# Optimization experiments

Hardware: AMD Instinct MI355X
Metric: run time of the kernel (lower is better)

Reference implementation:

```python
import jax, jax.numpy as jnp
import numpy as np

V = 500000        # total elements
S = 50000         # num samples (segments)
D = 128           # input = hidden = output size


def setup_inputs() -> dict:
    key = jax.random.key(0)
    k1, k2, k3, k4, k5 = jax.random.split(key, 5)
    scale = 1.0 / np.sqrt(D)
    return {
        "element_embeddings": jax.random.normal(k1, (V, D), dtype=jnp.float32),
        "element_to_sample_map": jnp.sort(jax.random.randint(k2, (V,), 0, S)),
        "num_samples": S,
        "Wq": jax.random.normal(k3, (D, D), dtype=jnp.float32) * scale,
        "Wk": jax.random.normal(k4, (D, D), dtype=jnp.float32) * scale,
        "Wo": jax.random.normal(k5, (D, D), dtype=jnp.float32) * scale,
    }


def reference(element_embeddings, element_to_sample_map, num_samples, Wq, Wk, Wo):
    x = element_embeddings                    # [V, D]
    idx = element_to_sample_map               # [V] int

    # --- query summarizer: linear projection + segment mean ---
    q_elem = x @ Wq.T                          # [V, H]
    q_sum = jax.ops.segment_sum(q_elem, idx, num_segments=num_samples)   # [S, H]
    counts = jax.ops.segment_sum(jnp.ones((x.shape[0],), x.dtype), idx,
                                 num_segments=num_samples)               # [S]
    queries = q_sum / jnp.maximum(counts, 1.0)[:, None]                  # [S, H]

    # --- attention scores: gather query per element, dot with key ---
    keys = x @ Wk.T                            # [V, H]
    queries_all = queries[idx]                 # [V, H] gather
    scores = jnp.einsum('vh,vh->v', queries_all, keys)                   # [V]

    # --- segment softmax (exp of scatter_log_softmax, eps=0) ---
    seg_max = jax.ops.segment_max(scores, idx, num_segments=num_samples) # [S]
    shifted = scores - seg_max[idx]
    e = jnp.exp(shifted)
    denom = jax.ops.segment_sum(e, idx, num_segments=num_samples)        # [S]
    probs = e / denom[idx]                                               # [V]

    # --- weighted scatter-sum of output projections ---
    out_elem = (x @ Wo.T) * probs[:, None]     # [V, D_out]
    return jax.ops.segment_sum(out_elem, idx, num_segments=num_samples)  # [S, D_out]
```

## Files before the change

kernel.cpp:

```cpp
#include <hip/hip_runtime.h>
#include <math.h>

#define D 128

__global__ void k_prep(const float* __restrict__ Wq, const float* __restrict__ Wk,
                       const float* __restrict__ Wo, float* __restrict__ M,
                       float* __restrict__ WoT) {
  int j = blockIdx.x, k = threadIdx.x;
  float acc = 0.f;
#pragma unroll 8
  for (int i = 0; i < D; ++i) acc = fmaf(Wq[i * D + j], Wk[i * D + k], acc);
  M[j * D + k] = acc;
  WoT[j * D + k] = Wo[k * D + j];
}

__global__ void k_starts(const int* __restrict__ idx, int* __restrict__ starts,
                         int V, int S) {
  int v = blockIdx.x * blockDim.x + threadIdx.x;
  if (v >= V) return;
  int c = idx[v];
  int p = (v == 0) ? -1 : idx[v - 1];
  for (int s = p + 1; s <= c; ++s) starts[s] = v;
  if (v == V - 1) {
    for (int s = c + 1; s <= S; ++s) starts[s] = V;
  }
}

__global__ void k_means(const float* __restrict__ x, const int* __restrict__ starts,
                        float* __restrict__ mean, int S) {
  int tid = blockIdx.x * blockDim.x + threadIdx.x;
  if (tid >= S * 32) return;
  int s = tid >> 5, g = tid & 31;
  int b = starts[s], e = starts[s + 1];
  float4 a = make_float4(0.f, 0.f, 0.f, 0.f);
  const float* xp = x + (size_t)b * D + g * 4;
  for (int v = b; v < e; ++v, xp += D) {
    float4 xv = *(const float4*)xp;
    a.x += xv.x; a.y += xv.y; a.z += xv.z; a.w += xv.w;
  }
  float inv = (e > b) ? 1.f / (float)(e - b) : 0.f;
  a.x *= inv; a.y *= inv; a.z *= inv; a.w *= inv;
  *(float4*)(mean + (size_t)s * D + g * 4) = a;
}

__global__ void k_rowmat4(const float* __restrict__ in, const float* __restrict__ B,
                          float* __restrict__ out, int S) {
  __shared__ float Bl[D * D];
  for (int i = threadIdx.x; i < D * D / 4; i += (int)blockDim.x)
    ((float4*)Bl)[i] = ((const float4*)B)[i];
  __syncthreads();
  int t = blockIdx.x * blockDim.x + threadIdx.x;
  int g = t & 31;
  int s0 = (t >> 5) * 4;
  if (s0 >= S) return;
  int nr = S - s0; nr = nr > 4 ? 4 : nr;
  float4 a0 = make_float4(0, 0, 0, 0), a1 = a0, a2 = a0, a3 = a0;
  const float4* r0 = (const float4*)(in + (size_t)s0 * D);
  const float4* r1 = (const float4*)(in + (size_t)(s0 + 1) * D);
  const float4* r2 = (const float4*)(in + (size_t)(s0 + 2) * D);
  const float4* r3 = (const float4*)(in + (size_t)(s0 + 3) * D);
#pragma unroll 4
  for (int j4 = 0; j4 < D / 4; ++j4) {
    float4 b0 = *(const float4*)(Bl + (j4 * 4 + 0) * D + g * 4);
    float4 b1 = *(const float4*)(Bl + (j4 * 4 + 1) * D + g * 4);
    float4 b2 = *(const float4*)(Bl + (j4 * 4 + 2) * D + g * 4);
    float4 b3 = *(const float4*)(Bl + (j4 * 4 + 3) * D + g * 4);
#define ROWFMA(ar, rr)                                                   \
    {                                                                    \
      float4 m = rr[j4];                                                 \
      ar.x = fmaf(m.x, b0.x, ar.x); ar.y = fmaf(m.x, b0.y, ar.y);        \
      ar.z = fmaf(m.x, b0.z, ar.z); ar.w = fmaf(m.x, b0.w, ar.w);        \
      ar.x = fmaf(m.y, b1.x, ar.x); ar.y = fmaf(m.y, b1.y, ar.y);        \
      ar.z = fmaf(m.y, b1.z, ar.z); ar.w = fmaf(m.y, b1.w, ar.w);        \
      ar.x = fmaf(m.z, b2.x, ar.x); ar.y = fmaf(m.z, b2.y, ar.y);        \
      ar.z = fmaf(m.z, b2.z, ar.z); ar.w = fmaf(m.z, b2.w, ar.w);        \
      ar.x = fmaf(m.w, b3.x, ar.x); ar.y = fmaf(m.w, b3.y, ar.y);        \
      ar.z = fmaf(m.w, b3.z, ar.z); ar.w = fmaf(m.w, b3.w, ar.w);        \
    }
    ROWFMA(a0, r0);
    if (nr > 1) ROWFMA(a1, r1);
    if (nr > 2) ROWFMA(a2, r2);
    if (nr > 3) ROWFMA(a3, r3);
#undef ROWFMA
  }
  *(float4*)(out + (size_t)s0 * D + g * 4) = a0;
  if (nr > 1) *(float4*)(out + (size_t)(s0 + 1) * D + g * 4) = a1;
  if (nr > 2) *(float4*)(out + (size_t)(s0 + 2) * D + g * 4) = a2;
  if (nr > 3) *(float4*)(out + (size_t)(s0 + 3) * D + g * 4) = a3;
}

__global__ void k_score_y(const float* __restrict__ x, const int* __restrict__ starts,
                          const float* __restrict__ t, float* __restrict__ y, int S) {
  int tid = blockIdx.x * blockDim.x + threadIdx.x;
  if (tid >= S * 32) return;
  int s = tid >> 5, g = tid & 31;
  int b = starts[s], e = starts[s + 1];
  float4 t4 = *(const float4*)(t + (size_t)s * D + g * 4);
  float4 a = make_float4(0.f, 0.f, 0.f, 0.f);
  float den = 0.f;
  const float* xp = x + (size_t)b * D + g * 4;
  for (int v = b; v < e; ++v, xp += D) {
    float4 xv = *(const float4*)xp;
    float p = t4.x * xv.x + t4.y * xv.y + t4.z * xv.z + t4.w * xv.w;
    p += __shfl_xor(p, 16);
    p += __shfl_xor(p, 8);
    p += __shfl_xor(p, 4);
    p += __shfl_xor(p, 2);
    p += __shfl_xor(p, 1);
    float w = __expf(p);
    den += w;
    a.x = fmaf(w, xv.x, a.x); a.y = fmaf(w, xv.y, a.y);
    a.z = fmaf(w, xv.z, a.z); a.w = fmaf(w, xv.w, a.w);
  }
  float inv = (den > 0.f) ? 1.f / den : 0.f;
  a.x *= inv; a.y *= inv; a.z *= inv; a.w *= inv;
  *(float4*)(y + (size_t)s * D + g * 4) = a;
}

extern "C" void kernel_launch(void* const* d_in, const int* in_sizes, int n_in,
                              void* d_out, int out_size, void* d_ws, size_t ws_size,
                              hipStream_t stream) {
  const float* x = (const float*)d_in[0];
  const int* idx = (const int*)d_in[1];
  const float* Wq = (const float*)d_in[3];
  const float* Wk = (const float*)d_in[4];
  const float* Wo = (const float*)d_in[5];
  float* out = (float*)d_out;
  const int V = in_sizes[1];
  const int S = out_size / D;

  char* ws = (char*)d_ws;
  float* M = (float*)(ws + 0);
  float* WoT = (float*)(ws + 65536);
  int* starts = (int*)(ws + 131072);
  size_t base = (131072 + 4 * (size_t)(S + 1) + 255) & ~(size_t)255;
  size_t segbytes = (size_t)S * D * 4;
  float* mean = (float*)(ws + base);
  float* y = mean;
  float* t = (float*)(ws + base + segbytes);

  hipLaunchKernelGGL(k_prep, dim3(D), dim3(D), 0, stream, Wq, Wk, Wo, M, WoT);
  hipLaunchKernelGGL(k_starts, dim3((V + 255) / 256), dim3(256), 0, stream, idx, starts, V, S);
  hipLaunchKernelGGL(k_means, dim3((S * 32 + 255) / 256), dim3(256), 0, stream, x, starts, mean, S);
  hipLaunchKernelGGL(k_rowmat4, dim3(((S + 3) / 4 * 32 + 255) / 256), dim3(256), 0, stream, mean, M, t, S);
  hipLaunchKernelGGL(k_score_y, dim3((S * 32 + 255) / 256), dim3(256), 0, stream, x, starts, t, y, S);
  hipLaunchKernelGGL(k_rowmat4, dim3(((S + 3) / 4 * 32 + 255) / 256), dim3(256), 0, stream, y, WoT, out, S);
}
```

Baseline: 273.2 us.

## Replace per-segment reduction kernels with element-tiled shared-memory segment sums

The per-segment kernels (one 32-lane group per segment looping over its elements) become an element-tiled kernel. Each block takes 64 consecutive rows, reduces them into shared-memory bins per segment, then writes interior segments directly and boundary segments with global atomics. Normalisation by count or softmax denominator moves into the epilogue of the row-matrix kernel, and a zeroing kernel is added for the accumulators. The aim is to remove the load imbalance and poor occupancy of variable-length segment loops. In exchange it adds atomics, an extra zeroing pass, and drops the max-shift from the softmax as before.

New measurement: 418.7 us. 1.53x slower.

```diff
diff --git a/kernel.cpp b/kernel.cpp
--- a/kernel.cpp
+++ b/kernel.cpp
@@ -2,6 +2,8 @@
 #include <math.h>
 
 #define D 128
+#define TR 64
+#define TPB 256
 
 __global__ void k_prep(const float* __restrict__ Wq, const float* __restrict__ Wk,
                        const float* __restrict__ Wo, float* __restrict__ M,
@@ -26,25 +28,139 @@
   }
 }
 
-__global__ void k_means(const float* __restrict__ x, const int* __restrict__ starts,
-                        float* __restrict__ mean, int S) {
-  int tid = blockIdx.x * blockDim.x + threadIdx.x;
-  if (tid >= S * 32) return;
-  int s = tid >> 5, g = tid & 31;
-  int b = starts[s], e = starts[s + 1];
-  float4 a = make_float4(0.f, 0.f, 0.f, 0.f);
-  const float* xp = x + (size_t)b * D + g * 4;
-  for (int v = b; v < e; ++v, xp += D) {
-    float4 xv = *(const float4*)xp;
-    a.x += xv.x; a.y += xv.y; a.z += xv.z; a.w += xv.w;
-  }
-  float inv = (e > b) ? 1.f / (float)(e - b) : 0.f;
-  a.x *= inv; a.y *= inv; a.z *= inv; a.w *= inv;
-  *(float4*)(mean + (size_t)s * D + g * 4) = a;
-}
-
+__global__ void k_zero(float4* __restrict__ p, long long nf4) {
+  long long i = (long long)blockIdx.x * blockDim.x + threadIdx.x;
+  long long st = (long long)gridDim.x * blockDim.x;
+  float4 z = make_float4(0.f, 0.f, 0.f, 0.f);
+  for (; i < nf4; i += st) p[i] = z;
+}
+
+template <int PASS>
+__global__ __launch_bounds__(TPB) void k_segsum(
+    const float* __restrict__ x, const int* __restrict__ idx,
+    const float* __restrict__ t, float* __restrict__ gout,
+    float* __restrict__ gden, int V) {
+  __shared__ float bsum[TR * D];
+  __shared__ float bden[TR];
+  __shared__ int brank[TR];
+  __shared__ int bseg[TR];
+  __shared__ int bnb;
+
+  const int tid = threadIdx.x;
+  const int wave = tid >> 6;
+  const int lane = tid & 63;
+  const int gl = lane & 31;
+  const int half = lane >> 5;
+  const int v0 = blockIdx.x * TR;
+  const int nrows = min(TR, V - v0);
+
+  if (wave == 0) {
+    int l = lane;
+    int seg = idx[v0 + min(l, nrows - 1)];
+    int prev = __shfl_up(seg, 1);
+    bool flag = (l > 0) && (l < nrows) && (seg != prev);
+    unsigned long long bal = __ballot(flag);
+    int rank = __popcll(bal << (63 - l));
+    brank[l] = rank;
+    if (l == 0 || flag) bseg[rank] = seg;
+    if (l == 63) bnb = rank + 1;
+  }
+  __syncthreads();
+  const int nb = bnb;
+  for (int i = tid; i < nb * D; i += TPB) bsum[i] = 0.f;
+  if (PASS == 2) {
+    for (int i = tid; i < nb; i += TPB) bden[i] = 0.f;
+  }
+  __syncthreads();
+
+  const int r0 = wave * 16 + half;
+
+  float4 xr[8];
+#pragma unroll
+  for (int i = 0; i < 8; ++i) {
+    int rv = v0 + min(r0 + 2 * i, nrows - 1);
+    xr[i] = *(const float4*)(x + (size_t)rv * D + gl * 4);
+  }
+
+  int curRank = brank[r0];
+  float4 t4 = make_float4(0.f, 0.f, 0.f, 0.f);
+  if (PASS == 2) {
+    int seg = bseg[curRank];
+    t4 = *(const float4*)(t + (size_t)seg * D + gl * 4);
+  }
+  float4 acc = make_float4(0.f, 0.f, 0.f, 0.f);
+  float dacc = 0.f;
+
+#pragma unroll
+  for (int i = 0; i < 8; ++i) {
+    int r = r0 + 2 * i;
+    bool valid = (r < nrows);
+    int rk = brank[min(r, TR - 1)];
+    if (rk != curRank) {
+      float* bp = bsum + curRank * D + gl * 4;
+      unsafeAtomicAdd(bp + 0, acc.x);
+      unsafeAtomicAdd(bp + 1, acc.y);
+      unsafeAtomicAdd(bp + 2, acc.z);
+      unsafeAtomicAdd(bp + 3, acc.w);
+      if (PASS == 2 && gl == 0) unsafeAtomicAdd(&bden[curRank], dacc);
+      acc = make_float4(0.f, 0.f, 0.f, 0.f);
+      dacc = 0.f;
+      curRank = rk;
+      if (PASS == 2) {
+        int seg = bseg[rk];
+        t4 = *(const float4*)(t + (size_t)seg * D + gl * 4);
+      }
+    }
+    float w = valid ? 1.f : 0.f;
+    if (PASS == 2) {
+      float4 xv = xr[i];
+      float p = t4.x * xv.x + t4.y * xv.y + t4.z * xv.z + t4.w * xv.w;
+      p += __shfl_xor(p, 16);
+      p += __shfl_xor(p, 8);
+      p += __shfl_xor(p, 4);
+      p += __shfl_xor(p, 2);
+      p += __shfl_xor(p, 1);
+      w = valid ? __expf(p) : 0.f;
+      dacc += w;
+    }
+    acc.x = fmaf(w, xr[i].x, acc.x);
+    acc.y = fmaf(w, xr[i].y, acc.y);
+    acc.z = fmaf(w, xr[i].z, acc.z);
+    acc.w = fmaf(w, xr[i].w, acc.w);
+  }
+  {
+    float* bp = bsum + curRank * D + gl * 4;
+    unsafeAtomicAdd(bp + 0, acc.x);
+    unsafeAtomicAdd(bp + 1, acc.y);
+    unsafeAtomicAdd(bp + 2, acc.z);
+    unsafeAtomicAdd(bp + 3, acc.w);
+    if (PASS == 2 && gl == 0) unsafeAtomicAdd(&bden[curRank], dacc);
+  }
+  __syncthreads();
+
+  for (int i = tid; i < nb * D; i += TPB) {
+    int b = i >> 7;
+    int c = i & (D - 1);
+    int seg = bseg[b];
+    float val = bsum[i];
+    float* gp = gout + (size_t)seg * D + c;
+    if (b == 0 || b == nb - 1) unsafeAtomicAdd(gp, val);
+    else *gp = val;
+  }
+  if (PASS == 2) {
+    for (int b = tid; b < nb; b += TPB) {
+      int seg = bseg[b];
+      if (b == 0 || b == nb - 1) unsafeAtomicAdd(gden + seg, bden[b]);
+      else gden[seg] = bden[b];
+    }
+  }
+}
+
+template <int MODE>
 __global__ void k_rowmat4(const float* __restrict__ in, const float* __restrict__ B,
-                          float* __restrict__ out, int S) {
+                          float* __restrict__ out, int S,
+                          const int* __restrict__ starts,
+                          const float* __restrict__ den) {
   __shared__ float Bl[D * D];
   for (int i = threadIdx.x; i < D * D / 4; i += (int)blockDim.x)
     ((float4*)Bl)[i] = ((const float4*)B)[i];
@@ -53,7 +169,8 @@
   int g = t & 31;
   int s0 = (t >> 5) * 4;
   if (s0 >= S) return;
-  int nr = S - s0; nr = nr > 4 ? 4 : nr;
+  int nr = S - s0;
+  nr = nr > 4 ? 4 : nr;
   float4 a0 = make_float4(0, 0, 0, 0), a1 = a0, a2 = a0, a3 = a0;
   const float4* r0 = (const float4*)(in + (size_t)s0 * D);
   const float4* r1 = (const float4*)(in + (size_t)(s0 + 1) * D);
@@ -83,38 +200,26 @@
     if (nr > 3) ROWFMA(a3, r3);
 #undef ROWFMA
   }
+  float sc[4];
+#pragma unroll
+  for (int k = 0; k < 4; ++k) {
+    int s = s0 + (k < nr ? k : 0);
+    if (MODE == 0) {
+      int n = starts[s + 1] - starts[s];
+      sc[k] = 1.f / (float)(n > 1 ? n : 1);
+    } else {
+      float dn = den[s];
+      sc[k] = (dn > 0.f) ? 1.f / dn : 0.f;
+    }
+  }
+  a0.x *= sc[0]; a0.y *= sc[0]; a0.z *= sc[0]; a0.w *= sc[0];
+  a1.x *= sc[1]; a1.y *= sc[1]; a1.z *= sc[1]; a1.w *= sc[1];
+  a2.x *= sc[2]; a2.y *= sc[2]; a2.z *= sc[2]; a2.w *= sc[2];
+  a3.x *= sc[3]; a3.y *= sc[3]; a3.z *= sc[3]; a3.w *= sc[3];
   *(float4*)(out + (size_t)s0 * D + g * 4) = a0;
   if (nr > 1) *(float4*)(out + (size_t)(s0 + 1) * D + g * 4) = a1;
   if (nr > 2) *(float4*)(out + (size_t)(s0 + 2) * D + g * 4) = a2;
   if (nr > 3) *(float4*)(out + (size_t)(s0 + 3) * D + g * 4) = a3;
-}
-
-__global__ void k_score_y(const float* __restrict__ x, const int* __restrict__ starts,
-                          const float* __restrict__ t, float* __restrict__ y, int S) {
-  int tid = blockIdx.x * blockDim.x + threadIdx.x;
-  if (tid >= S * 32) return;
-  int s = tid >> 5, g = tid & 31;
-  int b = starts[s], e = starts[s + 1];
-  float4 t4 = *(const float4*)(t + (size_t)s * D + g * 4);
-  float4 a = make_float4(0.f, 0.f, 0.f, 0.f);
-  float den = 0.f;
-  const float* xp = x + (size_t)b * D + g * 4;
-  for (int v = b; v < e; ++v, xp += D) {
-    float4 xv = *(const float4*)xp;
-    float p = t4.x * xv.x + t4.y * xv.y + t4.z * xv.z + t4.w * xv.w;
-    p += __shfl_xor(p, 16);
-    p += __shfl_xor(p, 8);
-    p += __shfl_xor(p, 4);
-    p += __shfl_xor(p, 2);
-    p += __shfl_xor(p, 1);
-    float w = __expf(p);
-    den += w;
-    a.x = fmaf(w, xv.x, a.x); a.y = fmaf(w, xv.y, a.y);
-    a.z = fmaf(w, xv.z, a.z); a.w = fmaf(w, xv.w, a.w);
-  }
-  float inv = (den > 0.f) ? 1.f / den : 0.f;
-  a.x *= inv; a.y *= inv; a.z *= inv; a.w *= inv;
-  *(float4*)(y + (size_t)s * D + g * 4) = a;
 }
 
 extern "C" void kernel_launch(void* const* d_in, const int* in_sizes, int n_in,
@@ -134,15 +239,20 @@
   float* WoT = (float*)(ws + 65536);
   int* starts = (int*)(ws + 131072);
   size_t base = (131072 + 4 * (size_t)(S + 1) + 255) & ~(size_t)255;
-  size_t segbytes = (size_t)S * D * 4;
-  float* mean = (float*)(ws + base);
-  float* y = mean;
-  float* t = (float*)(ws + base + segbytes);
+  float* qsum = (float*)(ws + base);
+  float* ysum = qsum + (size_t)S * D;
+  float* den = ysum + (size_t)S * D;
+  long long zf4 = ((long long)S * (2 * D + 1)) / 4;
+  size_t tbase = (base + (size_t)S * (2 * D + 1) * 4 + 255) & ~(size_t)255;
+  float* t = (float*)(ws + tbase);
+
+  const int NT = (V + TR - 1) / TR;
 
   hipLaunchKernelGGL(k_prep, dim3(D), dim3(D), 0, stream, Wq, Wk, Wo, M, WoT);
   hipLaunchKernelGGL(k_starts, dim3((V + 255) / 256), dim3(256), 0, stream, idx, starts, V, S);
-  hipLaunchKernelGGL(k_means, dim3((S * 32 + 255) / 256), dim3(256), 0, stream, x, starts, mean, S);
-  hipLaunchKernelGGL(k_rowmat4, dim3(((S + 3) / 4 * 32 + 255) / 256), dim3(256), 0, stream, mean, M, t, S);
-  hipLaunchKernelGGL(k_score_y, dim3((S * 32 + 255) / 256), dim3(256), 0, stream, x, starts, t, y, S);
-  hipLaunchKernelGGL(k_rowmat4, dim3(((S + 3) / 4 * 32 + 255) / 256), dim3(256), 0, stream, y, WoT, out, S);
-}
+  hipLaunchKernelGGL(k_zero, dim3(2048), dim3(256), 0, stream, (float4*)qsum, zf4);
+  hipLaunchKernelGGL((k_segsum<1>), dim3(NT), dim3(TPB), 0, stream, x, idx, (const float*)nullptr, qsum, (float*)nullptr, V);
+  hipLaunchKernelGGL((k_rowmat4<0>), dim3(((S + 3) / 4 * 32 + 255) / 256), dim3(256), 0, stream, qsum, M, t, S, starts, (const float*)nullptr);
+  hipLaunchKernelGGL((k_segsum<2>), dim3(NT), dim3(TPB), 0, stream, x, idx, t, ysum, den, V);
+  hipLaunchKernelGGL((k_rowmat4<1>), dim3(((S + 3) / 4 * 32 + 255) / 256), dim3(256), 0, stream, ysum, WoT, out, S, (const int*)nullptr, den);
+}
```

## Replace per-segment thread mapping with fixed row-chunk waves and boundary atomics

Applied to the files above, without the earlier changes.

Drops the segment-start computation and the per-segment loops. Each wave now processes a fixed chunk of 64 rows, finds segment boundaries with a ballot, and writes interior segments directly while using atomics for segments that cross chunk edges. Normalization by count or denominator moves into the epilogue of the row-matrix kernels. The goal is balanced work independent of segment lengths and no starts array, at the cost of an extra zeroing pass and atomic traffic at chunk boundaries.

After: 298.1 us. +9.1%, slower.

```diff
diff --git a/kernel.cpp b/kernel.cpp
--- a/kernel.cpp
+++ b/kernel.cpp
@@ -2,6 +2,9 @@
 #include <math.h>
 
 #define D 128
+#define RPW 64
+#define WPB 4
+#define RPB (RPW * WPB)
 
 __global__ void k_prep(const float* __restrict__ Wq, const float* __restrict__ Wk,
                        const float* __restrict__ Wo, float* __restrict__ M,
@@ -14,37 +17,92 @@
   WoT[j * D + k] = Wo[k * D + j];
 }
 
-__global__ void k_starts(const int* __restrict__ idx, int* __restrict__ starts,
-                         int V, int S) {
-  int v = blockIdx.x * blockDim.x + threadIdx.x;
-  if (v >= V) return;
-  int c = idx[v];
-  int p = (v == 0) ? -1 : idx[v - 1];
-  for (int s = p + 1; s <= c; ++s) starts[s] = v;
-  if (v == V - 1) {
-    for (int s = c + 1; s <= S; ++s) starts[s] = V;
-  }
+__global__ void k_zero(float4* __restrict__ p, long long nf4) {
+  long long i = (long long)blockIdx.x * blockDim.x + threadIdx.x;
+  long long st = (long long)gridDim.x * blockDim.x;
+  float4 z = make_float4(0.f, 0.f, 0.f, 0.f);
+  for (; i < nf4; i += st) p[i] = z;
 }
 
-__global__ void k_means(const float* __restrict__ x, const int* __restrict__ starts,
-                        float* __restrict__ mean, int S) {
-  int tid = blockIdx.x * blockDim.x + threadIdx.x;
-  if (tid >= S * 32) return;
-  int s = tid >> 5, g = tid & 31;
-  int b = starts[s], e = starts[s + 1];
-  float4 a = make_float4(0.f, 0.f, 0.f, 0.f);
-  const float* xp = x + (size_t)b * D + g * 4;
-  for (int v = b; v < e; ++v, xp += D) {
-    float4 xv = *(const float4*)xp;
-    a.x += xv.x; a.y += xv.y; a.z += xv.z; a.w += xv.w;
+template <int PASS>
+__global__ __launch_bounds__(256) void k_segsum(
+    const float* __restrict__ x, const int* __restrict__ idx,
+    const float* __restrict__ t, float* __restrict__ gout,
+    float* __restrict__ gden, int V) {
+  const int lane = threadIdx.x & 63;
+  const int wave = threadIdx.x >> 6;
+  const int r0 = blockIdx.x * RPB + wave * RPW;
+  if (r0 >= V) return;
+
+  const int myIdx = idx[min(r0 + lane, V - 1)];
+  const int prevIdx = __shfl_up(myIdx, 1);
+  const unsigned long long chg = __ballot(lane > 0 && myIdx != prevIdx);
+
+  const float* xw = x + (size_t)r0 * D + lane * 2;
+  float2 acc = make_float2(0.f, 0.f);
+  float dacc = 0.f;
+  int curSeg = __shfl(myIdx, 0);
+  int runStart = 0;
+  float2 t2 = make_float2(0.f, 0.f);
+  if (PASS == 2) t2 = *(const float2*)(t + (size_t)curSeg * D + lane * 2);
+
+#pragma unroll
+  for (int c = 0; c < RPW / 8; ++c) {
+    float2 xr[8];
+#pragma unroll
+    for (int j = 0; j < 8; ++j) {
+      int rr = min(r0 + c * 8 + j, V - 1) - r0;
+      xr[j] = *(const float2*)(xw + (size_t)rr * D);
+    }
+#pragma unroll
+    for (int j = 0; j < 8; ++j) {
+      const int i = c * 8 + j;
+      const bool valid = (r0 + i) < V;
+      if (i > 0 && ((chg >> i) & 1ull)) {
+        float* gp = gout + (size_t)curSeg * D + lane * 2;
+        if (runStart > 0) {
+          gp[0] = acc.x;
+          gp[1] = acc.y;
+          if (lane == 0) gden[curSeg] = dacc;
+        } else {
+          unsafeAtomicAdd(gp + 0, acc.x);
+          unsafeAtomicAdd(gp + 1, acc.y);
+          if (lane == 0) unsafeAtomicAdd(gden + curSeg, dacc);
+        }
+        acc = make_float2(0.f, 0.f);
+        dacc = 0.f;
+        curSeg = __shfl(myIdx, i);
+        runStart = i;
+        if (PASS == 2) t2 = *(const float2*)(t + (size_t)curSeg * D + lane * 2);
+      }
+      float w;
+      if (PASS == 1) {
+        w = valid ? 1.f : 0.f;
+      } else {
+        float p = t2.x * xr[j].x + t2.y * xr[j].y;
+        p += __shfl_xor(p, 32);
+        p += __shfl_xor(p, 16);
+        p += __shfl_xor(p, 8);
+        p += __shfl_xor(p, 4);
+        p += __shfl_xor(p, 2);
+        p += __shfl_xor(p, 1);
+        w = valid ? __expf(p) : 0.f;
+      }
+      acc.x = fmaf(w, xr[j].x, acc.x);
+      acc.y = fmaf(w, xr[j].y, acc.y);
+      dacc += w;
+    }
   }
-  float inv = (e > b) ? 1.f / (float)(e - b) : 0.f;
-  a.x *= inv; a.y *= inv; a.z *= inv; a.w *= inv;
-  *(float4*)(mean + (size_t)s * D + g * 4) = a;
+  float* gp = gout + (size_t)curSeg * D + lane * 2;
+  unsafeAtomicAdd(gp + 0, acc.x);
+  unsafeAtomicAdd(gp + 1, acc.y);
+  if (lane == 0) unsafeAtomicAdd(gden + curSeg, dacc);
 }
 
+template <int MODE>
 __global__ void k_rowmat4(const float* __restrict__ in, const float* __restrict__ B,
-                          float* __restrict__ out, int S) {
+                          float* __restrict__ out, int S,
+                          const float* __restrict__ den) {
   __shared__ float Bl[D * D];
   for (int i = threadIdx.x; i < D * D / 4; i += (int)blockDim.x)
     ((float4*)Bl)[i] = ((const float4*)B)[i];
@@ -53,7 +111,8 @@
   int g = t & 31;
   int s0 = (t >> 5) * 4;
   if (s0 >= S) return;
-  int nr = S - s0; nr = nr > 4 ? 4 : nr;
+  int nr = S - s0;
+  nr = nr > 4 ? 4 : nr;
   float4 a0 = make_float4(0, 0, 0, 0), a1 = a0, a2 = a0, a3 = a0;
   const float4* r0 = (const float4*)(in + (size_t)s0 * D);
   const float4* r1 = (const float4*)(in + (size_t)(s0 + 1) * D);
@@ -83,38 +142,22 @@
     if (nr > 3) ROWFMA(a3, r3);
 #undef ROWFMA
   }
+  float sc[4];
+#pragma unroll
+  for (int k = 0; k < 4; ++k) {
+    int s = s0 + (k < nr ? k : 0);
+    float dn = den[s];
+    if (MODE == 0) sc[k] = 1.f / fmaxf(dn, 1.f);
+    else sc[k] = (dn > 0.f) ? 1.f / dn : 0.f;
+  }
+  a0.x *= sc[0]; a0.y *= sc[0]; a0.z *= sc[0]; a0.w *= sc[0];
+  a1.x *= sc[1]; a1.y *= sc[1]; a1.z *= sc[1]; a1.w *= sc[1];
+  a2.x *= sc[2]; a2.y *= sc[2]; a2.z *= sc[2]; a2.w *= sc[2];
+  a3.x *= sc[3]; a3.y *= sc[3]; a3.z *= sc[3]; a3.w *= sc[3];
   *(float4*)(out + (size_t)s0 * D + g * 4) = a0;
   if (nr > 1) *(float4*)(out + (size_t)(s0 + 1) * D + g * 4) = a1;
   if (nr > 2) *(float4*)(out + (size_t)(s0 + 2) * D + g * 4) = a2;
   if (nr > 3) *(float4*)(out + (size_t)(s0 + 3) * D + g * 4) = a3;
-}
-
-__global__ void k_score_y(const float* __restrict__ x, const int* __restrict__ starts,
-                          const float* __restrict__ t, float* __restrict__ y, int S) {
-  int tid = blockIdx.x * blockDim.x + threadIdx.x;
-  if (tid >= S * 32) return;
-  int s = tid >> 5, g = tid & 31;
-  int b = starts[s], e = starts[s + 1];
-  float4 t4 = *(const float4*)(t + (size_t)s * D + g * 4);
-  float4 a = make_float4(0.f, 0.f, 0.f, 0.f);
-  float den = 0.f;
-  const float* xp = x + (size_t)b * D + g * 4;
-  for (int v = b; v < e; ++v, xp += D) {
-    float4 xv = *(const float4*)xp;
-    float p = t4.x * xv.x + t4.y * xv.y + t4.z * xv.z + t4.w * xv.w;
-    p += __shfl_xor(p, 16);
-    p += __shfl_xor(p, 8);
-    p += __shfl_xor(p, 4);
-    p += __shfl_xor(p, 2);
-    p += __shfl_xor(p, 1);
-    float w = __expf(p);
-    den += w;
-    a.x = fmaf(w, xv.x, a.x); a.y = fmaf(w, xv.y, a.y);
-    a.z = fmaf(w, xv.z, a.z); a.w = fmaf(w, xv.w, a.w);
-  }
-  float inv = (den > 0.f) ? 1.f / den : 0.f;
-  a.x *= inv; a.y *= inv; a.z *= inv; a.w *= inv;
-  *(float4*)(y + (size_t)s * D + g * 4) = a;
 }
 
 extern "C" void kernel_launch(void* const* d_in, const int* in_sizes, int n_in,
@@ -132,17 +175,23 @@
   char* ws = (char*)d_ws;
   float* M = (float*)(ws + 0);
   float* WoT = (float*)(ws + 65536);
-  int* starts = (int*)(ws + 131072);
-  size_t base = (131072 + 4 * (size_t)(S + 1) + 255) & ~(size_t)255;
-  size_t segbytes = (size_t)S * D * 4;
-  float* mean = (float*)(ws + base);
-  float* y = mean;
-  float* t = (float*)(ws + base + segbytes);
+  size_t base = 131072;
+  float* qsum = (float*)(ws + base);
+  float* ysum = qsum + (size_t)S * D;
+  float* cnt = ysum + (size_t)S * D;
+  float* den = cnt + S;
+  long long zf4 = ((long long)S * (2 * D + 2)) / 4;
+  size_t tbase = (base + (size_t)S * (2 * D + 2) * 4 + 255) & ~(size_t)255;
+  float* t = (float*)(ws + tbase);
+
+  const int NT = (V + RPB - 1) / RPB;
+  const int rmBlocks = ((S + 3) / 4 * 32 + 255) / 256;
 
   hipLaunchKernelGGL(k_prep, dim3(D), dim3(D), 0, stream, Wq, Wk, Wo, M, WoT);
-  hipLaunchKernelGGL(k_starts, dim3((V + 255) / 256), dim3(256), 0, stream, idx, starts, V, S);
-  hipLaunchKernelGGL(k_means, dim3((S * 32 + 255) / 256), dim3(256), 0, stream, x, starts, mean, S);
-  hipLaunchKernelGGL(k_rowmat4, dim3(((S + 3) / 4 * 32 + 255) / 256), dim3(256), 0, stream, mean, M, t, S);
-  hipLaunchKernelGGL(k_score_y, dim3((S * 32 + 255) / 256), dim3(256), 0, stream, x, starts, t, y, S);
-  hipLaunchKernelGGL(k_rowmat4, dim3(((S + 3) / 4 * 32 + 255) / 256), dim3(256), 0, stream, y, WoT, out, S);
+  hipLaunchKernelGGL(k_zero, dim3(2048), dim3(256), 0, stream, (float4*)qsum, zf4);
+  hipLaunchKernelGGL((k_segsum<1>), dim3(NT), dim3(256), 0, stream, x, idx,
+                     (const float*)nullptr, qsum, cnt, V);
+  hipLaunchKernelGGL((k_rowmat4<0>), dim3(rmBlocks), dim3(256), 0, stream, qsum, M, t, S, cnt);
+  hipLaunchKernelGGL((k_segsum<2>), dim3(NT), dim3(256), 0, stream, x, idx, t, ysum, den, V);
+  hipLaunchKernelGGL((k_rowmat4<1>), dim3(rmBlocks), dim3(256), 0, stream, ysum, WoT, out, S, den);
 }
```
